# Performance work log

Hardware: AMD Instinct MI355X
Metric: run time of the kernel (lower is better)

The kernel has to match this reference:

```python
import jax, jax.numpy as jnp
import numpy as np

B, T, D = 4, 2048, 1024
N, H = 16, 64          # num_heads, key_dim = D // N
F = 4096               # intermediate_dim
SOFT_CAP = 50.0
EPS = 1e-6


def layer_norm(x, gamma, beta, eps=EPS):
    mean = jnp.mean(x, axis=-1, keepdims=True)
    var = jnp.var(x, axis=-1, keepdims=True)
    return (x - mean) * jax.lax.rsqrt(var + eps) * gamma + beta


def setup_inputs() -> dict:
    key = jax.random.key(0)
    ks = jax.random.split(key, 16)
    s = 0.02
    return {
        "inputs": jax.random.normal(ks[0], (B, T, D), dtype=jnp.float32),
        "ln1_gamma": jnp.ones((D,), jnp.float32),
        "ln1_beta": jnp.zeros((D,), jnp.float32),
        "wq": jax.random.normal(ks[1], (D, N, H), jnp.float32) * s,
        "bq": jnp.zeros((N, H), jnp.float32),
        "wk": jax.random.normal(ks[2], (D, N, H), jnp.float32) * s,
        "bk": jnp.zeros((N, H), jnp.float32),
        "wv": jax.random.normal(ks[3], (D, N, H), jnp.float32) * s,
        "bv": jnp.zeros((N, H), jnp.float32),
        "wo": jax.random.normal(ks[4], (N, H, D), jnp.float32) * s,
        "bo": jnp.zeros((D,), jnp.float32),
        "ln2_gamma": jnp.ones((D,), jnp.float32),
        "ln2_beta": jnp.zeros((D,), jnp.float32),
        "w1": jax.random.normal(ks[5], (D, F), jnp.float32) * s,
        "b1": jax.random.normal(ks[6], (F,), jnp.float32) * 1e-6,
        "w2": jax.random.normal(ks[7], (F, D), jnp.float32) * s,
        "b2": jax.random.normal(ks[8], (D,), jnp.float32) * 1e-6,
    }


def reference(inputs, ln1_gamma, ln1_beta, wq, bq, wk, bk, wv, bv, wo, bo,
              ln2_gamma, ln2_beta, w1, b1, w2, b2):
    # --- pre-norm attention branch ---
    x = layer_norm(inputs, ln1_gamma, ln1_beta)
    q = jnp.einsum('btd,dnh->btnh', x, wq) + bq
    k = jnp.einsum('btd,dnh->btnh', x, wk) + bk
    v = jnp.einsum('btd,dnh->btnh', x, wv) + bv
    q = q * (1.0 / jnp.sqrt(jnp.float32(H)))
    score = jnp.einsum('btnh,bsnh->bnts', q, k)          # [B,N,T,T]
    score = SOFT_CAP * jnp.tanh(score / SOFT_CAP)        # logit soft cap
    weights = jax.nn.softmax(score.astype(jnp.float32), axis=-1).astype(q.dtype)
    context = jnp.einsum('bnts,bsnh->btnh', weights, v)
    attn_out = jnp.einsum('btnh,nhd->btd', context, wo) + bo
    x_res = attn_out + inputs
    # --- pre-norm MLP branch ---
    y = layer_norm(x_res, ln2_gamma, ln2_beta)
    y = jax.nn.gelu(y @ w1 + b1, approximate=False)
    y = y @ w2 + b2
    return x_res + y
```

## Files before the change

### kernel.cpp

```cpp
#include <hip/hip_runtime.h>
#include <hip/hip_bf16.h>
#include <math.h>

typedef __attribute__((ext_vector_type(8))) short short8;
typedef __attribute__((ext_vector_type(4))) short short4v;
typedef __attribute__((ext_vector_type(4))) float f32x4;

#define GAS __attribute__((address_space(1)))
#define LAS __attribute__((address_space(3)))

__device__ __forceinline__ LAS void* to_lds(void* p) {
    return (LAS void*)(unsigned)(uintptr_t)p;
}

constexpr int Bc = 4, Tc = 2048, Dc = 1024, Nheads = 16, Hc = 64, Fc = 4096;
constexpr int Mrows = Bc * Tc;
constexpr float LNEPS = 1e-6f;

__device__ __forceinline__ float gelu_exact(float x) {
    return 0.5f * x * (1.0f + erff(x * 0.70710678118654752440f));
}

__global__ __launch_bounds__(256) void transpose_cvt(const float* __restrict__ src,
                                                     __hip_bfloat16* __restrict__ dst,
                                                     int K, int N) {
    __shared__ float tile[32][33];
    const int n0 = blockIdx.x * 32, k0 = blockIdx.y * 32;
    const int tx = threadIdx.x & 31, ty = threadIdx.x >> 5;
    #pragma unroll
    for (int i = 0; i < 32; i += 8)
        tile[ty + i][tx] = src[(size_t)(k0 + ty + i) * N + (n0 + tx)];
    __syncthreads();
    #pragma unroll
    for (int i = 0; i < 32; i += 8)
        dst[(size_t)(n0 + ty + i) * K + (k0 + tx)] = __float2bfloat16(tile[tx][ty + i]);
}

__global__ __launch_bounds__(256) void transpose_v(const __hip_bfloat16* __restrict__ qkv,
                                                   __hip_bfloat16* __restrict__ vT) {
    __shared__ short tile[32][33];
    const int t0 = blockIdx.x * 32, h0 = blockIdx.y * 32, bn = blockIdx.z;
    const int b = bn >> 4, n = bn & 15;
    const short* src = (const short*)qkv + (size_t)b * Tc * 3072 + 2048 + n * 64;
    short* dst = (short*)vT + (size_t)bn * 64 * Tc;
    const int tx = threadIdx.x & 31, ty = threadIdx.x >> 5;
    #pragma unroll
    for (int i = 0; i < 32; i += 8)
        tile[ty + i][tx] = src[(size_t)(t0 + ty + i) * 3072 + h0 + tx];
    __syncthreads();
    #pragma unroll
    for (int i = 0; i < 32; i += 8)
        dst[(size_t)(h0 + ty + i) * Tc + t0 + tx] = tile[tx][ty + i];
}

__global__ void concat_bias(const float* __restrict__ bq, const float* __restrict__ bk,
                            const float* __restrict__ bv, float* __restrict__ dst) {
    int i = blockIdx.x * 256 + threadIdx.x;
    float v = (i < 1024) ? bq[i] : (i < 2048 ? bk[i - 1024] : bv[i - 2048]);
    dst[i] = v;
}

__global__ __launch_bounds__(256) void ln_kernel(const float* __restrict__ x,
                                                 const float* __restrict__ gamma,
                                                 const float* __restrict__ beta,
                                                 __hip_bfloat16* __restrict__ out) {
    __shared__ float2 red[4];
    const int row = blockIdx.x, tid = threadIdx.x;
    const float* xr = x + (size_t)row * Dc;
    float4 v = ((const float4*)xr)[tid];
    float s  = v.x + v.y + v.z + v.w;
    float ss = v.x * v.x + v.y * v.y + v.z * v.z + v.w * v.w;
    #pragma unroll
    for (int o = 32; o; o >>= 1) { s += __shfl_down(s, o, 64); ss += __shfl_down(ss, o, 64); }
    if ((tid & 63) == 0) red[tid >> 6] = make_float2(s, ss);
    __syncthreads();
    float2 r0 = red[0], r1 = red[1], r2 = red[2], r3 = red[3];
    s  = r0.x + r1.x + r2.x + r3.x;
    ss = r0.y + r1.y + r2.y + r3.y;
    const float mean = s * (1.0f / Dc);
    const float var  = ss * (1.0f / Dc) - mean * mean;
    const float inv  = rsqrtf(var + LNEPS);
    float4 g  = ((const float4*)gamma)[tid];
    float4 bb = ((const float4*)beta)[tid];
    __hip_bfloat16* orow = out + (size_t)row * Dc + tid * 4;
    orow[0] = __float2bfloat16((v.x - mean) * inv * g.x + bb.x);
    orow[1] = __float2bfloat16((v.y - mean) * inv * g.y + bb.y);
    orow[2] = __float2bfloat16((v.z - mean) * inv * g.z + bb.z);
    orow[3] = __float2bfloat16((v.w - mean) * inv * g.w + bb.w);
}

template <int EPI, bool OUT_BF16>
__global__ __launch_bounds__(256) void gemm_kernel(
    const __hip_bfloat16* __restrict__ A, const __hip_bfloat16* __restrict__ Bt,
    const float* __restrict__ bias, const float* __restrict__ resid,
    void* __restrict__ Cout, int M, int N, int K) {
    __shared__ __align__(16) short As[128 * 32];
    __shared__ __align__(16) short Bs[128 * 32];
    const int tid = threadIdx.x;
    const int wave = tid >> 6, lane = tid & 63, quad = lane >> 4, l16 = lane & 15;
    const int m0 = blockIdx.x * 128, n0 = blockIdx.y * 128;
    const int wm = (wave >> 1) * 64, wn = (wave & 1) * 64;
    f32x4 acc[4][4] = {};

    const int srow = wave * 16 + (lane >> 2);
    const int scol = (lane & 3) * 8;
    const short* aSrc0 = (const short*)A  + (size_t)(m0 + srow) * K + scol;
    const short* aSrc1 = aSrc0 + (size_t)64 * K;
    const short* bSrc0 = (const short*)Bt + (size_t)(n0 + srow) * K + scol;
    const short* bSrc1 = bSrc0 + (size_t)64 * K;
    LAS void* ldsA0 = to_lds(&As[(wave * 16) * 32]);
    LAS void* ldsA1 = to_lds(&As[(64 + wave * 16) * 32]);
    LAS void* ldsB0 = to_lds(&Bs[(wave * 16) * 32]);
    LAS void* ldsB1 = to_lds(&Bs[(64 + wave * 16) * 32]);

    for (int k0 = 0; k0 < K; k0 += 32) {
        __builtin_amdgcn_global_load_lds((const GAS void*)(aSrc0 + k0), ldsA0, 16, 0, 0);
        __builtin_amdgcn_global_load_lds((const GAS void*)(aSrc1 + k0), ldsA1, 16, 0, 0);
        __builtin_amdgcn_global_load_lds((const GAS void*)(bSrc0 + k0), ldsB0, 16, 0, 0);
        __builtin_amdgcn_global_load_lds((const GAS void*)(bSrc1 + k0), ldsB1, 16, 0, 0);
        __syncthreads();
        short8 af[4], bfr[4];
        #pragma unroll
        for (int i = 0; i < 4; i++) af[i]  = *(const short8*)&As[(wm + i * 16 + l16) * 32 + quad * 8];
        #pragma unroll
        for (int i = 0; i < 4; i++) bfr[i] = *(const short8*)&Bs[(wn + i * 16 + l16) * 32 + quad * 8];
        #pragma unroll
        for (int i = 0; i < 4; i++)
            #pragma unroll
            for (int j = 0; j < 4; j++)
                acc[i][j] = __builtin_amdgcn_mfma_f32_16x16x32_bf16(af[i], bfr[j], acc[i][j], 0, 0, 0);
        __syncthreads();
    }
    #pragma unroll
    for (int i = 0; i < 4; i++) {
        #pragma unroll
        for (int j = 0; j < 4; j++) {
            const int col = n0 + wn + j * 16 + l16;
            const float bv = bias[col];
            #pragma unroll
            for (int r = 0; r < 4; r++) {
                const int row = m0 + wm + i * 16 + quad * 4 + r;
                float val = acc[i][j][r] + bv;
                if (EPI == 1) val = gelu_exact(val);
                if (EPI == 2) val += resid[(size_t)row * N + col];
                if (OUT_BF16)
                    ((__hip_bfloat16*)Cout)[(size_t)row * N + col] = __float2bfloat16(val);
                else
                    ((float*)Cout)[(size_t)row * N + col] = val;
            }
        }
    }
}

template <int EPI, bool OUT_BF16>
__global__ __launch_bounds__(512, 2) void gemm256(
    const __hip_bfloat16* __restrict__ A, const __hip_bfloat16* __restrict__ Bt,
    const float* __restrict__ bias, const float* __restrict__ resid,
    void* __restrict__ Cout, int M, int N, int K) {
    __shared__ __align__(1024) short As[2][256 * 64];
    __shared__ __align__(1024) short Bs[2][256 * 64];
    const int tid = threadIdx.x;
    const int wave = tid >> 6, lane = tid & 63, quad = lane >> 4, l16 = lane & 15;
    const int wm = wave >> 2, wn = wave & 3;
    const int m0 = blockIdx.x * 256, n0 = blockIdx.y * 256;

    const int subrow = lane >> 3;
    const int scb = (((lane & 7) ^ subrow) << 4);
    const int arowb[4] = {0, 128, 64, 192};
    const int browb[4] = {0, 128, 32, 160};
    const char* aSrc[4]; const char* bSrc[4];
    int aLds[4], bLds[4];
    #pragma unroll
    for (int i = 0; i < 4; ++i) {
        const int rA = arowb[i] + wave * 8;
        aSrc[i] = (const char*)A + ((size_t)(m0 + rA + subrow) * K) * 2 + scb;
        aLds[i] = rA * 128;
        const int rB = browb[i] + (wave >> 2) * 64 + (wave & 3) * 8;
        bSrc[i] = (const char*)Bt + ((size_t)(n0 + rB + subrow) * K) * 2 + scb;
        bLds[i] = rB * 128;
    }
    const int nt = K >> 6;

    #define STG_A(i, tt, dstbuf) \
        __builtin_amdgcn_global_load_lds((const GAS void*)(aSrc[i] + (size_t)(tt) * 128), \
                                         to_lds((char*)&As[dstbuf][0] + aLds[i]), 16, 0, 0)
    #define STG_B(i, tt, dstbuf) \
        __builtin_amdgcn_global_load_lds((const GAS void*)(bSrc[i] + (size_t)(tt) * 128), \
                                         to_lds((char*)&Bs[dstbuf][0] + bLds[i]), 16, 0, 0)

    STG_A(0, 0, 0); STG_A(1, 0, 0);
    STG_B(0, 0, 0); STG_B(1, 0, 0);
    STG_B(2, 0, 0); STG_B(3, 0, 0);
    STG_A(2, 0, 0); STG_A(3, 0, 0);
    asm volatile("s_waitcnt vmcnt(4)\n\ts_barrier" ::: "memory");

    const int cb0 = ((quad ^ (l16 & 7)) << 4);
    const int cb1 = cb0 ^ 64;
    f32x4 acc[8][4] = {};

    for (int t = 0; t < nt; ++t) {
        const int cb = t & 1, nb = cb ^ 1;
        const char* Ard = (const char*)&As[cb][0] + (wm * 128 + l16) * 128;
        const char* Brd = (const char*)&Bs[cb][0] + (wn * 64 + l16) * 128;
        const bool stg = (t + 1 < nt);
        short8 af[4][2], bf[4][2];

        #pragma unroll
        for (int mi = 0; mi < 4; ++mi) {
            af[mi][0] = *(const short8*)(Ard + mi * 2048 + cb0);
            af[mi][1] = *(const short8*)(Ard + mi * 2048 + cb1);
        }
        #pragma unroll
        for (int nj = 0; nj < 2; ++nj) {
            bf[nj][0] = *(const short8*)(Brd + nj * 2048 + cb0);
            bf[nj][1] = *(const short8*)(Brd + nj * 2048 + cb1);
        }
        if (stg) {
            STG_A(0, t + 1, nb); STG_A(1, t + 1, nb);
            asm volatile("s_waitcnt vmcnt(4)\n\ts_barrier" ::: "memory");
        } else {
            asm volatile("s_waitcnt vmcnt(2)\n\ts_barrier" ::: "memory");
        }
        __builtin_amdgcn_s_setprio(1);
        #pragma unroll
        for (int mi = 0; mi < 4; ++mi)
            #pragma unroll
            for (int nj = 0; nj < 2; ++nj) {
                acc[mi][nj] = __builtin_amdgcn_mfma_f32_16x16x32_bf16(af[mi][0], bf[nj][0], acc[mi][nj], 0, 0, 0);
                acc[mi][nj] = __builtin_amdgcn_mfma_f32_16x16x32_bf16(af[mi][1], bf[nj][1], acc[mi][nj], 0, 0, 0);
            }
        __builtin_amdgcn_s_setprio(0);
        asm volatile("s_barrier" ::: "memory");

        #pragma unroll
        for (int nj = 2; nj < 4; ++nj) {
            bf[nj][0] = *(const short8*)(Brd + nj * 2048 + cb0);
            bf[nj][1] = *(const short8*)(Brd + nj * 2048 + cb1);
        }
        if (stg) {
            STG_B(0, t + 1, nb); STG_B(1, t + 1, nb);
            asm volatile("s_waitcnt vmcnt(4)\n\ts_barrier" ::: "memory");
        } else {
            asm volatile("s_waitcnt vmcnt(0)\n\ts_barrier" ::: "memory");
        }
        __builtin_amdgcn_s_setprio(1);
        #pragma unroll
        for (int mi = 0; mi < 4; ++mi)
            #pragma unroll
            for (int nj = 2; nj < 4; ++nj) {
                acc[mi][nj] = __builtin_amdgcn_mfma_f32_16x16x32_bf16(af[mi][0], bf[nj][0], acc[mi][nj], 0, 0, 0);
                acc[mi][nj] = __builtin_amdgcn_mfma_f32_16x16x32_bf16(af[mi][1], bf[nj][1], acc[mi][nj], 0, 0, 0);
            }
        __builtin_amdgcn_s_setprio(0);
        asm volatile("s_barrier" ::: "memory");

        #pragma unroll
        for (int mi = 0; mi < 4; ++mi) {
            af[mi][0] = *(const short8*)(Ard + (mi + 4) * 2048 + cb0);
            af[mi][1] = *(const short8*)(Ard + (mi + 4) * 2048 + cb1);
        }
        if (stg) { STG_B(2, t + 1, nb); STG_B(3, t + 1, nb); }
        asm volatile("s_barrier" ::: "memory");
        __builtin_amdgcn_s_setprio(1);
        #pragma unroll
        for (int mi = 0; mi < 4; ++mi)
            #pragma unroll
            for (int nj = 2; nj < 4; ++nj) {
                acc[mi + 4][nj] = __builtin_amdgcn_mfma_f32_16x16x32_bf16(af[mi][0], bf[nj][0], acc[mi + 4][nj], 0, 0, 0);
                acc[mi + 4][nj] = __builtin_amdgcn_mfma_f32_16x16x32_bf16(af[mi][1], bf[nj][1], acc[mi + 4][nj], 0, 0, 0);
            }
        __builtin_amdgcn_s_setprio(0);
        asm volatile("s_barrier" ::: "memory");

        if (stg) {
            STG_A(2, t + 1, nb); STG_A(3, t + 1, nb);
            asm volatile("s_waitcnt vmcnt(4)\n\ts_barrier" ::: "memory");
        } else {
            asm volatile("s_barrier" ::: "memory");
        }
        __builtin_amdgcn_s_setprio(1);
        #pragma unroll
        for (int mi = 0; mi < 4; ++mi)
            #pragma unroll
            for (int nj = 0; nj < 2; ++nj) {
                acc[mi + 4][nj] = __builtin_amdgcn_mfma_f32_16x16x32_bf16(af[mi][0], bf[nj][0], acc[mi + 4][nj], 0, 0, 0);
                acc[mi + 4][nj] = __builtin_amdgcn_mfma_f32_16x16x32_bf16(af[mi][1], bf[nj][1], acc[mi + 4][nj], 0, 0, 0);
            }
        __builtin_amdgcn_s_setprio(0);
        asm volatile("s_barrier" ::: "memory");
    }
    #undef STG_A
    #undef STG_B

    #pragma unroll
    for (int mi = 0; mi < 8; ++mi) {
        #pragma unroll
        for (int nj = 0; nj < 4; ++nj) {
            const int col = n0 + wn * 64 + nj * 16 + l16;
            const float bv = bias[col];
            #pragma unroll
            for (int r = 0; r < 4; ++r) {
                const int row = m0 + wm * 128 + mi * 16 + quad * 4 + r;
                float val = acc[mi][nj][r] + bv;
                if (EPI == 1) val = gelu_exact(val);
                if (EPI == 2) val += resid[(size_t)row * N + col];
                if (OUT_BF16)
                    ((__hip_bfloat16*)Cout)[(size_t)row * N + col] = __float2bfloat16(val);
                else
                    ((float*)Cout)[(size_t)row * N + col] = val;
            }
        }
    }
}

__global__ __launch_bounds__(512, 4) void flash_attn(const __hip_bfloat16* __restrict__ qkv,
                                                     const __hip_bfloat16* __restrict__ vT,
                                                     __hip_bfloat16* __restrict__ ctx) {
    constexpr int NHD = 3072;
    constexpr int LP = 72;
    __shared__ __align__(1024) short Ks[2][64 * 64];
    __shared__ __align__(1024) short Vs[2][64 * 64];
    __shared__ __align__(16) short Ps[8 * 32 * LP];

    const int tid = threadIdx.x;
    const int wave = tid >> 6, lane = tid & 63, quad = lane >> 4, l16 = lane & 15;
    const int wg = blockIdx.x;
    const int rb = (wg & 7) * 64 + (wg >> 3);
    const int bx = rb & 7, bn = rb >> 3;
    const int t0 = bx * 256;
    const int bb = bn >> 4, hn = bn & 15;
    const __hip_bfloat16* Qg  = qkv + ((size_t)(bb * Tc + t0)) * NHD + hn * Hc;
    const __hip_bfloat16* Kg  = qkv + (size_t)bb * Tc * NHD + Dc + hn * Hc;
    const __hip_bfloat16* vTg = vT + (size_t)bn * 64 * Tc;

    const int wm = wave * 32;
    short* Psw = Ps + wave * 32 * LP;

    short8 bq[2][2];
    #pragma unroll
    for (int kt = 0; kt < 2; ++kt)
        #pragma unroll
        for (int i = 0; i < 2; ++i)
            bq[kt][i] = *(const short8*)&Qg[(size_t)(wm + i * 16 + l16) * NHD + kt * 32 + quad * 8];

    const int srow = lane >> 3;
    const int scb = (((lane & 7) ^ srow) << 4);
    const char* kSrc = (const char*)Kg + (size_t)(wave * 8 + srow) * (NHD * 2) + scb;
    const char* vSrc = (const char*)vTg + (size_t)(wave * 8 + srow) * (Tc * 2) + scb;
    const int ldsOff = wave * 1024;

    #define STG_KV(tt, b) do { \
        __builtin_amdgcn_global_load_lds((const GAS void*)(kSrc + (size_t)(tt) * 64 * (NHD * 2)), \
                                         to_lds((char*)&Ks[b][0] + ldsOff), 16, 0, 0); \
        __builtin_amdgcn_global_load_lds((const GAS void*)(vSrc + (size_t)(tt) * 128), \
                                         to_lds((char*)&Vs[b][0] + ldsOff), 16, 0, 0); \
    } while (0)

    const short4v ONES4 = {0x3F80, 0x3F80, 0x3F80, 0x3F80};
    short8 ones;
    *(short4v*)&ones = ONES4;
    *((short4v*)&ones + 1) = ONES4;

    f32x4 o_acc[2][4] = {};
    f32x4 l_mf[2]  = {};

    constexpr float C0 = 0.125f;
    constexpr float C1 = -2.60416667e-7f;
    constexpr float C2 = 6.51041667e-13f;

    const int rslot0 = ((quad ^ (l16 & 7)) << 4);
    const int rslot1 = rslot0 ^ 64;

    STG_KV(0, 0);
    for (int t = 0; t < Tc / 64; ++t) {
        const int cb = t & 1;
        if (t + 1 < Tc / 64) {
            STG_KV(t + 1, cb ^ 1);
            asm volatile("s_waitcnt vmcnt(2)\n\ts_barrier" ::: "memory");
        } else {
            asm volatile("s_waitcnt vmcnt(0)\n\ts_barrier" ::: "memory");
        }
        const char* Kb = (const char*)&Ks[cb][0];
        const char* Vb = (const char*)&Vs[cb][0];

        #pragma unroll
        for (int jh = 0; jh < 2; ++jh) {
            f32x4 st[2][2] = {};
            #pragma unroll
            for (int kt = 0; kt < 2; ++kt) {
                short8 ak[2];
                #pragma unroll
                for (int jj = 0; jj < 2; ++jj)
                    ak[jj] = *(const short8*)(Kb + ((jh * 2 + jj) * 16 + l16) * 128 + (kt ? rslot1 : rslot0));
                __builtin_amdgcn_s_setprio(1);
                #pragma unroll
                for (int jj = 0; jj < 2; ++jj)
                    #pragma unroll
                    for (int i = 0; i < 2; ++i)
                        st[jj][i] = __builtin_amdgcn_mfma_f32_16x16x32_bf16(ak[jj], bq[kt][i], st[jj][i], 0, 0, 0);
                __builtin_amdgcn_s_setprio(0);
            }
            #pragma unroll
            for (int jj = 0; jj < 2; ++jj)
                #pragma unroll
                for (int i = 0; i < 2; ++i) {
                    union { short4v v; unsigned short u[4]; } pk;
                    #pragma unroll
                    for (int r = 0; r < 4; ++r) {
                        const float sc = st[jj][i][r];
                        const float u  = sc * sc;
                        float tt = sc * fmaf(fmaf(C2, u, C1), u, C0);
                        tt = fminf(tt, 60.0f);
                        const float p = __expf(tt);
                        __hip_bfloat16 h = __float2bfloat16(p);
                        pk.u[r] = __builtin_bit_cast(unsigned short, h);
                    }
                    *(short4v*)&Psw[(i * 16 + l16) * LP + (jh * 2 + jj) * 16 + quad * 4] = pk.v;
                }
        }
        asm volatile("" ::: "memory");

        #pragma unroll
        for (int kt = 0; kt < 2; ++kt) {
            short8 ap[2], bv_[4];
            #pragma unroll
            for (int i = 0; i < 2; ++i)
                ap[i] = *(const short8*)&Psw[(i * 16 + l16) * LP + kt * 32 + quad * 8];
            #pragma unroll
            for (int ht = 0; ht < 4; ++ht)
                bv_[ht] = *(const short8*)(Vb + (ht * 16 + l16) * 128 + (kt ? rslot1 : rslot0));
            __builtin_amdgcn_s_setprio(1);
            #pragma unroll
            for (int i = 0; i < 2; ++i)
                l_mf[i] = __builtin_amdgcn_mfma_f32_16x16x32_bf16(ap[i], ones, l_mf[i], 0, 0, 0);
            #pragma unroll
            for (int i = 0; i < 2; ++i)
                #pragma unroll
                for (int ht = 0; ht < 4; ++ht)
                    o_acc[i][ht] = __builtin_amdgcn_mfma_f32_16x16x32_bf16(ap[i], bv_[ht], o_acc[i][ht], 0, 0, 0);
            __builtin_amdgcn_s_setprio(0);
        }
        asm volatile("s_barrier" ::: "memory");
    }
    #undef STG_KV

    #pragma unroll
    for (int i = 0; i < 2; ++i) {
        float linv[4];
        #pragma unroll
        for (int r = 0; r < 4; ++r) linv[r] = 1.0f / l_mf[i][r];
        #pragma unroll
        for (int ht = 0; ht < 4; ++ht)
            #pragma unroll
            for (int r = 0; r < 4; ++r) {
                const int row = t0 + wm + i * 16 + quad * 4 + r;
                const int col = hn * Hc + ht * 16 + l16;
                ctx[((size_t)(bb * Tc + row)) * Dc + col] =
                    __float2bfloat16(o_acc[i][ht][r] * linv[r]);
            }
    }
}

extern "C" void kernel_launch(void* const* d_in, const int* in_sizes, int n_in,
                              void* d_out, int out_size, void* d_ws, size_t ws_size,
                              hipStream_t stream) {
    const float* inputs = (const float*)d_in[0];
    const float* ln1_g  = (const float*)d_in[1];
    const float* ln1_b  = (const float*)d_in[2];
    const float* wq     = (const float*)d_in[3];
    const float* bq     = (const float*)d_in[4];
    const float* wk     = (const float*)d_in[5];
    const float* bk     = (const float*)d_in[6];
    const float* wv     = (const float*)d_in[7];
    const float* bv     = (const float*)d_in[8];
    const float* wo     = (const float*)d_in[9];
    const float* bo     = (const float*)d_in[10];
    const float* ln2_g  = (const float*)d_in[11];
    const float* ln2_b  = (const float*)d_in[12];
    const float* w1     = (const float*)d_in[13];
    const float* b1     = (const float*)d_in[14];
    const float* w2     = (const float*)d_in[15];
    const float* b2     = (const float*)d_in[16];

    char* ws = (char*)d_ws;
    auto alloc = [&](size_t bytes) {
        char* p = ws;
        ws += (bytes + 255) & ~(size_t)255;
        return p;
    };
    __hip_bfloat16* wqkv_t = (__hip_bfloat16*)alloc((size_t)3072 * 1024 * 2);
    __hip_bfloat16* wo_t   = (__hip_bfloat16*)alloc((size_t)1024 * 1024 * 2);
    __hip_bfloat16* w1_t   = (__hip_bfloat16*)alloc((size_t)4096 * 1024 * 2);
    __hip_bfloat16* w2_t   = (__hip_bfloat16*)alloc((size_t)4096 * 1024 * 2);
    float*          bqkv   = (float*)alloc(3072 * 4);
    __hip_bfloat16* xn     = (__hip_bfloat16*)alloc((size_t)Mrows * 1024 * 2);
    __hip_bfloat16* qkv    = (__hip_bfloat16*)alloc((size_t)Mrows * 3072 * 2);
    __hip_bfloat16* vTr    = (__hip_bfloat16*)alloc((size_t)64 * 64 * Tc * 2);
    __hip_bfloat16* ctx    = (__hip_bfloat16*)alloc((size_t)Mrows * 1024 * 2);
    float*          xres   = (float*)alloc((size_t)Mrows * 1024 * 4);
    __hip_bfloat16* y1     = qkv;

    dim3 blk(256);
    transpose_cvt<<<dim3(32, 32), blk, 0, stream>>>(wq, wqkv_t, 1024, 1024);
    transpose_cvt<<<dim3(32, 32), blk, 0, stream>>>(wk, wqkv_t + 1024 * 1024, 1024, 1024);
    transpose_cvt<<<dim3(32, 32), blk, 0, stream>>>(wv, wqkv_t + 2048 * 1024, 1024, 1024);
    transpose_cvt<<<dim3(32, 32), blk, 0, stream>>>(wo, wo_t, 1024, 1024);
    transpose_cvt<<<dim3(128, 32), blk, 0, stream>>>(w1, w1_t, 1024, 4096);
    transpose_cvt<<<dim3(32, 128), blk, 0, stream>>>(w2, w2_t, 4096, 1024);
    concat_bias<<<dim3(12), blk, 0, stream>>>(bq, bk, bv, bqkv);

    ln_kernel<<<dim3(Mrows), blk, 0, stream>>>(inputs, ln1_g, ln1_b, xn);
    gemm256<0, true><<<dim3(32, 12), dim3(512), 0, stream>>>(xn, wqkv_t, bqkv, nullptr, qkv, Mrows, 3072, 1024);
    transpose_v<<<dim3(64, 2, 64), blk, 0, stream>>>(qkv, vTr);
    flash_attn<<<dim3(512), dim3(512), 0, stream>>>(qkv, vTr, ctx);
    gemm_kernel<2, false><<<dim3(64, 8), blk, 0, stream>>>(ctx, wo_t, bo, inputs, xres, Mrows, 1024, 1024);
    ln_kernel<<<dim3(Mrows), blk, 0, stream>>>(xres, ln2_g, ln2_b, xn);
    gemm256<1, true><<<dim3(32, 16), dim3(512), 0, stream>>>(xn, w1_t, b1, nullptr, y1, Mrows, 4096, 1024);
    gemm_kernel<2, false><<<dim3(64, 8), blk, 0, stream>>>(y1, w2_t, b2, xres, (float*)d_out, Mrows, 1024, 4096);
}
```

Measured before the change: 576.6 us.

## Replace simple 128x128 GEMM with pipelined 256x128 kernel for output projections

Adds a 256x128-tile GEMM variant of the double-buffered, swizzled, LDS-direct-load gemm256 pipeline. It replaces the simple single-buffered 128x128 gemm_kernel for the attention output projection and the MLP down-projection, both with N=1024. The aim is to overlap global loads with MFMA work and cut LDS bank conflicts on these two GEMMs. The narrower N tile keeps 256 blocks in the grid, which reduces wave-quantization issues but leaves fewer blocks than a 128x128 tiling would.

```diff
diff --git a/kernel.cpp b/kernel.cpp
--- a/kernel.cpp
+++ b/kernel.cpp
@@ -90,69 +90,6 @@
 }
 
 template <int EPI, bool OUT_BF16>
-__global__ __launch_bounds__(256) void gemm_kernel(
-    const __hip_bfloat16* __restrict__ A, const __hip_bfloat16* __restrict__ Bt,
-    const float* __restrict__ bias, const float* __restrict__ resid,
-    void* __restrict__ Cout, int M, int N, int K) {
-    __shared__ __align__(16) short As[128 * 32];
-    __shared__ __align__(16) short Bs[128 * 32];
-    const int tid = threadIdx.x;
-    const int wave = tid >> 6, lane = tid & 63, quad = lane >> 4, l16 = lane & 15;
-    const int m0 = blockIdx.x * 128, n0 = blockIdx.y * 128;
-    const int wm = (wave >> 1) * 64, wn = (wave & 1) * 64;
-    f32x4 acc[4][4] = {};
-
-    const int srow = wave * 16 + (lane >> 2);
-    const int scol = (lane & 3) * 8;
-    const short* aSrc0 = (const short*)A  + (size_t)(m0 + srow) * K + scol;
-    const short* aSrc1 = aSrc0 + (size_t)64 * K;
-    const short* bSrc0 = (const short*)Bt + (size_t)(n0 + srow) * K + scol;
-    const short* bSrc1 = bSrc0 + (size_t)64 * K;
-    LAS void* ldsA0 = to_lds(&As[(wave * 16) * 32]);
-    LAS void* ldsA1 = to_lds(&As[(64 + wave * 16) * 32]);
-    LAS void* ldsB0 = to_lds(&Bs[(wave * 16) * 32]);
-    LAS void* ldsB1 = to_lds(&Bs[(64 + wave * 16) * 32]);
-
-    for (int k0 = 0; k0 < K; k0 += 32) {
-        __builtin_amdgcn_global_load_lds((const GAS void*)(aSrc0 + k0), ldsA0, 16, 0, 0);
-        __builtin_amdgcn_global_load_lds((const GAS void*)(aSrc1 + k0), ldsA1, 16, 0, 0);
-        __builtin_amdgcn_global_load_lds((const GAS void*)(bSrc0 + k0), ldsB0, 16, 0, 0);
-        __builtin_amdgcn_global_load_lds((const GAS void*)(bSrc1 + k0), ldsB1, 16, 0, 0);
-        __syncthreads();
-        short8 af[4], bfr[4];
-        #pragma unroll
-        for (int i = 0; i < 4; i++) af[i]  = *(const short8*)&As[(wm + i * 16 + l16) * 32 + quad * 8];
-        #pragma unroll
-        for (int i = 0; i < 4; i++) bfr[i] = *(const short8*)&Bs[(wn + i * 16 + l16) * 32 + quad * 8];
-        #pragma unroll
-        for (int i = 0; i < 4; i++)
-            #pragma unroll
-            for (int j = 0; j < 4; j++)
-                acc[i][j] = __builtin_amdgcn_mfma_f32_16x16x32_bf16(af[i], bfr[j], acc[i][j], 0, 0, 0);
-        __syncthreads();
-    }
-    #pragma unroll
-    for (int i = 0; i < 4; i++) {
-        #pragma unroll
-        for (int j = 0; j < 4; j++) {
-            const int col = n0 + wn + j * 16 + l16;
-            const float bv = bias[col];
-            #pragma unroll
-            for (int r = 0; r < 4; r++) {
-                const int row = m0 + wm + i * 16 + quad * 4 + r;
-                float val = acc[i][j][r] + bv;
-                if (EPI == 1) val = gelu_exact(val);
-                if (EPI == 2) val += resid[(size_t)row * N + col];
-                if (OUT_BF16)
-                    ((__hip_bfloat16*)Cout)[(size_t)row * N + col] = __float2bfloat16(val);
-                else
-                    ((float*)Cout)[(size_t)row * N + col] = val;
-            }
-        }
-    }
-}
-
-template <int EPI, bool OUT_BF16>
 __global__ __launch_bounds__(512, 2) void gemm256(
     const __hip_bfloat16* __restrict__ A, const __hip_bfloat16* __restrict__ Bt,
     const float* __restrict__ bias, const float* __restrict__ resid,
@@ -297,6 +234,153 @@
         #pragma unroll
         for (int nj = 0; nj < 4; ++nj) {
             const int col = n0 + wn * 64 + nj * 16 + l16;
+            const float bv = bias[col];
+            #pragma unroll
+            for (int r = 0; r < 4; ++r) {
+                const int row = m0 + wm * 128 + mi * 16 + quad * 4 + r;
+                float val = acc[mi][nj][r] + bv;
+                if (EPI == 1) val = gelu_exact(val);
+                if (EPI == 2) val += resid[(size_t)row * N + col];
+                if (OUT_BF16)
+                    ((__hip_bfloat16*)Cout)[(size_t)row * N + col] = __float2bfloat16(val);
+                else
+                    ((float*)Cout)[(size_t)row * N + col] = val;
+            }
+        }
+    }
+}
+
+template <int EPI, bool OUT_BF16>
+__global__ __launch_bounds__(512, 2) void gemm256x128(
+    const __hip_bfloat16* __restrict__ A, const __hip_bfloat16* __restrict__ Bt,
+    const float* __restrict__ bias, const float* __restrict__ resid,
+    void* __restrict__ Cout, int M, int N, int K) {
+    __shared__ __align__(1024) short As[2][256 * 64];
+    __shared__ __align__(1024) short Bs[2][128 * 64];
+    const int tid = threadIdx.x;
+    const int wave = tid >> 6, lane = tid & 63, quad = lane >> 4, l16 = lane & 15;
+    const int wm = wave >> 2, wn = wave & 3;
+    const int m0 = blockIdx.x * 256, n0 = blockIdx.y * 128;
+
+    const int subrow = lane >> 3;
+    const int scb = (((lane & 7) ^ subrow) << 4);
+    const int arowb[4] = {0, 128, 64, 192};
+    const char* aSrc[4]; int aLds[4];
+    #pragma unroll
+    for (int i = 0; i < 4; ++i) {
+        const int rA = arowb[i] + wave * 8;
+        aSrc[i] = (const char*)A + ((size_t)(m0 + rA + subrow) * K) * 2 + scb;
+        aLds[i] = rA * 128;
+    }
+    const char* bSrc[2]; int bLds[2];
+    #pragma unroll
+    for (int i = 0; i < 2; ++i) {
+        const int rB = (wave >> 1) * 32 + (wave & 1) * 8 + i * 16;
+        bSrc[i] = (const char*)Bt + ((size_t)(n0 + rB + subrow) * K) * 2 + scb;
+        bLds[i] = rB * 128;
+    }
+    const int nt = K >> 6;
+
+    #define STG_A(i, tt, dstbuf) \
+        __builtin_amdgcn_global_load_lds((const GAS void*)(aSrc[i] + (size_t)(tt) * 128), \
+                                         to_lds((char*)&As[dstbuf][0] + aLds[i]), 16, 0, 0)
+    #define STG_B(i, tt, dstbuf) \
+        __builtin_amdgcn_global_load_lds((const GAS void*)(bSrc[i] + (size_t)(tt) * 128), \
+                                         to_lds((char*)&Bs[dstbuf][0] + bLds[i]), 16, 0, 0)
+
+    STG_A(0, 0, 0); STG_A(1, 0, 0);
+    STG_B(0, 0, 0); STG_B(1, 0, 0);
+    STG_A(2, 0, 0); STG_A(3, 0, 0);
+    asm volatile("s_waitcnt vmcnt(3)\n\ts_barrier" ::: "memory");
+
+    const int cb0 = ((quad ^ (l16 & 7)) << 4);
+    const int cb1 = cb0 ^ 64;
+    f32x4 acc[8][2] = {};
+
+    for (int t = 0; t < nt; ++t) {
+        const int cb = t & 1, nb = cb ^ 1;
+        const char* Ard = (const char*)&As[cb][0] + (wm * 128 + l16) * 128;
+        const char* Brd = (const char*)&Bs[cb][0] + (wn * 32 + l16) * 128;
+        const bool stg = (t + 1 < nt);
+        short8 af[4][2], bf[2][2];
+
+        #pragma unroll
+        for (int mi = 0; mi < 4; ++mi) {
+            af[mi][0] = *(const short8*)(Ard + mi * 2048 + cb0);
+            af[mi][1] = *(const short8*)(Ard + mi * 2048 + cb1);
+        }
+        bf[0][0] = *(const short8*)(Brd + cb0);
+        bf[0][1] = *(const short8*)(Brd + cb1);
+        if (stg) {
+            STG_A(0, t + 1, nb); STG_A(1, t + 1, nb);
+            asm volatile("s_waitcnt vmcnt(4)\n\ts_barrier" ::: "memory");
+        } else {
+            asm volatile("s_waitcnt vmcnt(2)\n\ts_barrier" ::: "memory");
+        }
+        __builtin_amdgcn_s_setprio(1);
+        #pragma unroll
+        for (int mi = 0; mi < 4; ++mi) {
+            acc[mi][0] = __builtin_amdgcn_mfma_f32_16x16x32_bf16(af[mi][0], bf[0][0], acc[mi][0], 0, 0, 0);
+            acc[mi][0] = __builtin_amdgcn_mfma_f32_16x16x32_bf16(af[mi][1], bf[0][1], acc[mi][0], 0, 0, 0);
+        }
+        __builtin_amdgcn_s_setprio(0);
+        asm volatile("s_barrier" ::: "memory");
+
+        bf[1][0] = *(const short8*)(Brd + 2048 + cb0);
+        bf[1][1] = *(const short8*)(Brd + 2048 + cb1);
+        if (stg) {
+            STG_B(0, t + 1, nb); STG_B(1, t + 1, nb);
+            asm volatile("s_waitcnt vmcnt(4)\n\ts_barrier" ::: "memory");
+        } else {
+            asm volatile("s_waitcnt vmcnt(0)\n\ts_barrier" ::: "memory");
+        }
+        __builtin_amdgcn_s_setprio(1);
+        #pragma unroll
+        for (int mi = 0; mi < 4; ++mi) {
+            acc[mi][1] = __builtin_amdgcn_mfma_f32_16x16x32_bf16(af[mi][0], bf[1][0], acc[mi][1], 0, 0, 0);
+            acc[mi][1] = __builtin_amdgcn_mfma_f32_16x16x32_bf16(af[mi][1], bf[1][1], acc[mi][1], 0, 0, 0);
+        }
+        __builtin_amdgcn_s_setprio(0);
+        asm volatile("s_barrier" ::: "memory");
+
+        #pragma unroll
+        for (int mi = 0; mi < 4; ++mi) {
+            af[mi][0] = *(const short8*)(Ard + (mi + 4) * 2048 + cb0);
+            af[mi][1] = *(const short8*)(Ard + (mi + 4) * 2048 + cb1);
+        }
+        if (stg) { STG_A(2, t + 1, nb); STG_A(3, t + 1, nb); }
+        asm volatile("s_barrier" ::: "memory");
+        __builtin_amdgcn_s_setprio(1);
+        #pragma unroll
+        for (int mi = 0; mi < 4; ++mi) {
+            acc[mi + 4][1] = __builtin_amdgcn_mfma_f32_16x16x32_bf16(af[mi][0], bf[1][0], acc[mi + 4][1], 0, 0, 0);
+            acc[mi + 4][1] = __builtin_amdgcn_mfma_f32_16x16x32_bf16(af[mi][1], bf[1][1], acc[mi + 4][1], 0, 0, 0);
+        }
+        __builtin_amdgcn_s_setprio(0);
+        asm volatile("s_barrier" ::: "memory");
+
+        if (stg) {
+            asm volatile("s_waitcnt vmcnt(2)\n\ts_barrier" ::: "memory");
+        } else {
+            asm volatile("s_barrier" ::: "memory");
+        }
+        __builtin_amdgcn_s_setprio(1);
+        #pragma unroll
+        for (int mi = 0; mi < 4; ++mi) {
+            acc[mi + 4][0] = __builtin_amdgcn_mfma_f32_16x16x32_bf16(af[mi][0], bf[0][0], acc[mi + 4][0], 0, 0, 0);
+            acc[mi + 4][0] = __builtin_amdgcn_mfma_f32_16x16x32_bf16(af[mi][1], bf[0][1], acc[mi + 4][0], 0, 0, 0);
+        }
+        __builtin_amdgcn_s_setprio(0);
+        asm volatile("s_barrier" ::: "memory");
+    }
+    #undef STG_A
+    #undef STG_B
+
+    #pragma unroll
+    for (int mi = 0; mi < 8; ++mi) {
+        #pragma unroll
+        for (int nj = 0; nj < 2; ++nj) {
+            const int col = n0 + wn * 32 + nj * 16 + l16;
             const float bv = bias[col];
             #pragma unroll
             for (int r = 0; r < 4; ++r) {
@@ -513,8 +597,8 @@
     gemm256<0, true><<<dim3(32, 12), dim3(512), 0, stream>>>(xn, wqkv_t, bqkv, nullptr, qkv, Mrows, 3072, 1024);
     transpose_v<<<dim3(64, 2, 64), blk, 0, stream>>>(qkv, vTr);
     flash_attn<<<dim3(512), dim3(512), 0, stream>>>(qkv, vTr, ctx);
-    gemm_kernel<2, false><<<dim3(64, 8), blk, 0, stream>>>(ctx, wo_t, bo, inputs, xres, Mrows, 1024, 1024);
+    gemm256x128<2, false><<<dim3(32, 8), dim3(512), 0, stream>>>(ctx, wo_t, bo, inputs, xres, Mrows, 1024, 1024);
     ln_kernel<<<dim3(Mrows), blk, 0, stream>>>(xres, ln2_g, ln2_b, xn);
     gemm256<1, true><<<dim3(32, 16), dim3(512), 0, stream>>>(xn, w1_t, b1, nullptr, y1, Mrows, 4096, 1024);
-    gemm_kernel<2, false><<<dim3(64, 8), blk, 0, stream>>>(y1, w2_t, b2, xres, (float*)d_out, Mrows, 1024, 4096);
-}
+    gemm256x128<2, false><<<dim3(32, 8), dim3(512), 0, stream>>>(y1, w2_t, b2, xres, (float*)d_out, Mrows, 1024, 4096);
+}
```

New measurement: 545.2 us, median of 3. 1.06x faster.
